# Kernel optimization log

Hardware: AMD Instinct MI355X
Metric: run time of the kernel (lower is better)

The kernel has to match this reference:

```python
import jax, jax.numpy as jnp
import numpy as np

CAPS_N, DIMS_N, ROUNDS = 10, 16, 3
IN_CAPS_N, IN_DIMS_N = 1152, 8
BATCH = 256
EPS = 1e-7  # keras backend.epsilon()


def squash(x, axis=-1):
    sq = jnp.sum(x * x, axis=axis, keepdims=True)
    return (sq / (1.0 + sq)) * x / jnp.sqrt(sq + EPS)


def setup_inputs() -> dict:
    key = jax.random.key(0)
    k1, k2 = jax.random.split(key)
    inputs = jax.random.normal(k1, (BATCH, IN_CAPS_N, IN_DIMS_N), dtype=jnp.float32)
    # glorot-ish scale for the transform weights
    W = jax.random.normal(k2, (CAPS_N, IN_CAPS_N, DIMS_N, IN_DIMS_N), dtype=jnp.float32) * 0.05
    return {"inputs": inputs, "W": W}


def reference(inputs, W):
    # u_hat[b,j,i,d] = W[j,i] @ inputs[b,i]  (per-pair prediction vectors)
    u_hat = jnp.einsum('jide,bie->bjid', W, inputs)  # [B, caps_n, in_caps_n, dims_n]
    B = inputs.shape[0]
    cc = jnp.zeros((B, CAPS_N, IN_CAPS_N), dtype=u_hat.dtype)  # routing logits
    v = None
    for r in range(ROUNDS):
        c = jax.nn.softmax(cc, axis=1)                    # softmax over output capsules
        s = jnp.einsum('bji,bjid->bjd', c, u_hat)         # weighted sum over input caps
        v = squash(s, axis=-1)                            # [B, caps_n, dims_n]
        if r != ROUNDS - 1:
            cc = cc + jnp.einsum('bjid,bjd->bji', u_hat, v)  # agreement
    return v
```

## Files before the change

### kernel.cpp

```cpp
#include <hip/hip_runtime.h>

#define B_N 256
#define IC_N 1152
#define J_N 10
#define D_N 16

typedef __attribute__((ext_vector_type(8))) short short8;
typedef __attribute__((ext_vector_type(4))) float floatx4;

union u4s8 { uint4 u; short8 s; };

__device__ __forceinline__ float bf_lo(unsigned int u){
  union { unsigned int i; float f; } c; c.i = u << 16; return c.f;
}
__device__ __forceinline__ float bf_hi(unsigned int u){
  union { unsigned int i; float f; } c; c.i = u & 0xffff0000u; return c.f;
}
__device__ __forceinline__ unsigned int rne16(float f){
  union { float ff; unsigned int i; } c; c.ff = f;
  return (c.i + 0x7FFFu + ((c.i >> 16) & 1u)) >> 16;
}
__device__ __forceinline__ unsigned int pack_rne(float lo, float hi){
  return rne16(lo) | (rne16(hi) << 16);
}
__device__ __forceinline__ unsigned int pack_trunc(float lo, float hi){
  union { float f; unsigned int u; } a, b; a.f = lo; b.f = hi;
  return __builtin_amdgcn_perm(b.u, a.u, 0x07060302u);
}

__global__ __launch_bounds__(256) void caps_prep(
    const float* __restrict__ W, uint4* __restrict__ wsf,
    uint4* __restrict__ wcc2, float* __restrict__ vsum)
{
  const int tid = threadIdx.x;
  const int t0 = blockIdx.x * 256 + tid;
  if (t0 < B_N * J_N * D_N) vsum[t0] = 0.f;
  __shared__ unsigned int lw[1024];
  const int j = blockIdx.x / 72, itile = blockIdx.x % 72;
  const float4* Wt = (const float4*)(W + ((size_t)(j * IC_N + itile * 16) << 7));
  #pragma unroll
  for (int h = 0; h < 2; ++h) {
    const float4 f = Wt[h * 256 + tid];
    lw[(h * 256 + tid) * 2]     = pack_rne(f.x, f.y);
    lw[(h * 256 + tid) * 2 + 1] = pack_rne(f.z, f.w);
  }
  __syncthreads();
  {
    const int ktl = tid >> 6, ln = tid & 63;
    const int base = (ktl * 4 + (ln >> 4)) * 64 + (ln & 15) * 4;
    uint4 q;
    q.x = lw[base]; q.y = lw[base + 1]; q.z = lw[base + 2]; q.w = lw[base + 3];
    wsf[((size_t)j * 288 + itile * 4 + ktl) * 64 + ln] = q;
  }
  {
    const int e = tid >> 5, lane2 = tid & 31;
    const int il = lane2 & 15, dbase = (lane2 >> 4) * 8;
    unsigned short h[8];
    #pragma unroll
    for (int k = 0; k < 8; ++k) {
      const unsigned int u = lw[il * 64 + (dbase + k) * 4 + (e >> 1)];
      h[k] = (e & 1) ? (unsigned short)(u >> 16) : (unsigned short)(u & 0xffffu);
    }
    uint4 q;
    q.x = h[0] | ((unsigned int)h[1] << 16);
    q.y = h[2] | ((unsigned int)h[3] << 16);
    q.z = h[4] | ((unsigned int)h[5] << 16);
    q.w = h[6] | ((unsigned int)h[7] << 16);
    wcc2[(((size_t)j * 8 + e) * 72 + itile) * 32 + lane2] = q;
  }
}

__global__ __launch_bounds__(640, 5) void caps_pass(
    const float* __restrict__ x,
    const uint4* __restrict__ wsf, const uint4* __restrict__ wcc2,
    const uint4* __restrict__ vsbf, float* __restrict__ s_part, const int round)
{
  __shared__ float ccl[10 * 32 * 17];
  __shared__ unsigned int xt[32 * 17 * 4];

  const int tid  = threadIdx.x;
  const int wave = tid >> 6;
  const int lane = tid & 63;
  const int quad = lane >> 4;
  const int col  = lane & 15;
  const int b0   = blockIdx.x << 4;
  const int i0   = blockIdx.y << 5;

  if (tid < 512) {
    const int b = tid >> 5, j4 = tid & 31;
    const int half = j4 & 1;
    #pragma unroll
    for (int ii = 0; ii < 2; ++ii) {
      const int i = ii * 16 + (j4 >> 1);
      const float4 v = ((const float4*)(x + ((size_t)((b0 + b) * IC_N + i0 + i) << 3)))[half];
      const int idx = ((i * 17 + b) << 2) + (half << 1);
      xt[idx]     = pack_rne(v.x, v.y);
      xt[idx + 1] = pack_rne(v.z, v.w);
    }
  }
  __syncthreads();
  const uint4* xtq = (const uint4*)xt;

  if (round > 0) {
    short8 av = {0,0,0,0,0,0,0,0};
    if (quad < 2)
      av = *(const short8*)&vsbf[((size_t)(b0 + col) * J_N + wave) * 2 + quad];
    #pragma unroll
    for (int c = 0; c < 2; ++c) {
      uint4 bvq[8];
      #pragma unroll
      for (int e = 0; e < 8; ++e) {
        uint4 q = {0u, 0u, 0u, 0u};
        if (lane < 32)
          q = wcc2[(((size_t)wave * 8 + e) * 72 + (blockIdx.y * 2 + c)) * 32 + lane];
        bvq[e] = q;
      }
      uint4 xr[4];
      #pragma unroll
      for (int r = 0; r < 4; ++r)
        xr[r] = xtq[(c * 16 + col) * 17 + quad * 4 + r];
      floatx4 cc4 = {0.f, 0.f, 0.f, 0.f};
      #pragma unroll
      for (int e = 0; e < 8; ++e) {
        u4s8 bv; bv.u = bvq[e];
        floatx4 tf = {0.f, 0.f, 0.f, 0.f};
        tf = __builtin_amdgcn_mfma_f32_16x16x32_bf16(av, bv.s, tf, 0, 0, 0);
        #pragma unroll
        for (int r = 0; r < 4; ++r) {
          const unsigned int u = ((const unsigned int*)&xr[r])[e >> 1];
          const float xe = (e & 1) ? bf_hi(u) : bf_lo(u);
          cc4[r] += tf[r] * xe;
        }
      }
      #pragma unroll
      for (int r = 0; r < 4; ++r)
        ccl[(wave * 32 + c * 16 + col) * 17 + quad * 4 + r] = cc4[r];
    }
    __syncthreads();
    if (tid < 512) {
      const int i = tid >> 4, b = tid & 15;
      float cc[10];
      #pragma unroll
      for (int j = 0; j < 10; ++j) cc[j] = ccl[(j * 32 + i) * 17 + b];
      float m = cc[0];
      #pragma unroll
      for (int j = 1; j < 10; ++j) m = fmaxf(m, cc[j]);
      float den = 0.f;
      #pragma unroll
      for (int j = 0; j < 10; ++j) { cc[j] = __expf(cc[j] - m); den += cc[j]; }
      const float rd = __builtin_amdgcn_rcpf(den);
      #pragma unroll
      for (int j = 0; j < 10; ++j) ccl[(j * 32 + i) * 17 + b] = cc[j] * rd;
    }
    __syncthreads();
  }

  floatx4 acc = {0.f, 0.f, 0.f, 0.f};
  #pragma unroll
  for (int kt = 0; kt < 8; ++kt) {
    const int il = kt * 4 + quad;
    const uint4 xq = xtq[il * 17 + col];
    const uint4 wf = wsf[((size_t)wave * 288 + (blockIdx.y << 3) + kt) * 64 + lane];
    const float c = (round > 0) ? ccl[(wave * 32 + il) * 17 + col] : 0.1f;
    short8 af;
    unsigned int* aq = (unsigned int*)&af;
    aq[0] = pack_trunc(bf_lo(xq.x) * c, bf_hi(xq.x) * c);
    aq[1] = pack_trunc(bf_lo(xq.y) * c, bf_hi(xq.y) * c);
    aq[2] = pack_trunc(bf_lo(xq.z) * c, bf_hi(xq.z) * c);
    aq[3] = pack_trunc(bf_lo(xq.w) * c, bf_hi(xq.w) * c);
    u4s8 bw; bw.u = wf;
    acc = __builtin_amdgcn_mfma_f32_16x16x32_bf16(af, bw.s, acc, 0, 0, 0);
  }
  float* sp = s_part + ((((size_t)blockIdx.x * 10 + wave) * 16 + quad * 4) * 36
                        + blockIdx.y) * 16 + col;
  #pragma unroll
  for (int r = 0; r < 4; ++r) sp[(size_t)r * 36 * 16] = acc[r];
}

__global__ __launch_bounds__(256) void caps_squash(
    const float* __restrict__ s_part, float* __restrict__ vsum,
    unsigned int* __restrict__ vsbf_u, float* __restrict__ out, const int round)
{
  const int tid  = threadIdx.x;
  const int w    = tid >> 6;
  const int lane = tid & 63;
  const int bj   = blockIdx.x * 4 + w;
  const int b    = bj / 10, j = bj - b * 10;
  const int btile = b >> 4, brem = b & 15;
  const float* base = s_part + (((size_t)btile * 10 + j) * 16 + brem) * 576;
  float acc = 0.f;
  #pragma unroll
  for (int q = 0; q < 9; ++q) acc += base[q * 64 + lane];
  acc += __shfl_xor(acc, 16, 64);
  acc += __shfl_xor(acc, 32, 64);
  const float s = acc;
  float sq = s * s;
  sq += __shfl_xor(sq, 1, 16);
  sq += __shfl_xor(sq, 2, 16);
  sq += __shfl_xor(sq, 4, 16);
  sq += __shfl_xor(sq, 8, 16);
  const float coef = (sq / (1.f + sq)) * rsqrtf(sq + 1e-7f);
  const float v = coef * s;
  if (round < 2) {
    const float vprev = (lane < 16) ? vsum[bj * 16 + lane] : 0.f;
    const float vt = vprev + v;
    const float vtn = __shfl_down(vt, 1, 64);
    if (lane < 16) {
      vsum[bj * 16 + lane] = vt;
      if (!(lane & 1))
        vsbf_u[bj * 8 + (lane >> 1)] = pack_rne(vt, vtn);
    }
  } else if (lane < 16) {
    out[bj * 16 + lane] = v;
  }
}

extern "C" void kernel_launch(void* const* d_in, const int* in_sizes, int n_in,
                              void* d_out, int out_size, void* d_ws, size_t ws_size,
                              hipStream_t stream)
{
  const float* x_p = (const float*)d_in[0];
  const float* W_p = (const float*)d_in[1];

  uint4* wsf   = (uint4*)d_ws;
  uint4* wcc2  = wsf + 184320;
  float* s_prt = (float*)(wcc2 + 184320);
  float* vsum  = s_prt + 2949120;
  unsigned int* vsbf_u = (unsigned int*)(vsum + 40960);
  float* out_p = (float*)d_out;

  caps_prep<<<dim3(720), dim3(256), 0, stream>>>(W_p, wsf, wcc2, vsum);
  for (int r = 0; r < 3; ++r) {
    caps_pass<<<dim3(16, 36), dim3(640), 0, stream>>>(
        x_p, wsf, wcc2, (const uint4*)vsbf_u, s_prt, r);
    caps_squash<<<dim3(640), dim3(256), 0, stream>>>(
        s_prt, vsum, vsbf_u, out_p, r);
  }
}
```

Before: 111.3 us.

## Fuse squash into next routing pass and drop intermediate squash launches

Each routing pass now reduces the previous round's partial sums and applies squash itself, building the bf16 agreement operand in shared memory. This removes two intermediate squash kernels and the vsbf staging buffer. Ping-pong partial-sum buffers separate the rounds, and vsum is written once by the blockIdx.y==0 blocks. The cost is that every one of the 36 i-tile blocks redundantly re-reads and re-reduces the same 16x10 slab of partial sums, which greatly increases cache traffic and adds latency before the main MFMA work.

```diff
diff --git a/kernel.cpp b/kernel.cpp
--- a/kernel.cpp
+++ b/kernel.cpp
@@ -30,11 +30,9 @@
 
 __global__ __launch_bounds__(256) void caps_prep(
     const float* __restrict__ W, uint4* __restrict__ wsf,
-    uint4* __restrict__ wcc2, float* __restrict__ vsum)
+    uint4* __restrict__ wcc2)
 {
   const int tid = threadIdx.x;
-  const int t0 = blockIdx.x * 256 + tid;
-  if (t0 < B_N * J_N * D_N) vsum[t0] = 0.f;
   __shared__ unsigned int lw[1024];
   const int j = blockIdx.x / 72, itile = blockIdx.x % 72;
   const float4* Wt = (const float4*)(W + ((size_t)(j * IC_N + itile * 16) << 7));
@@ -73,10 +71,12 @@
 __global__ __launch_bounds__(640, 5) void caps_pass(
     const float* __restrict__ x,
     const uint4* __restrict__ wsf, const uint4* __restrict__ wcc2,
-    const uint4* __restrict__ vsbf, float* __restrict__ s_part, const int round)
+    const float* __restrict__ sp_prev, float* __restrict__ sp_cur,
+    float* __restrict__ vsum, const int round)
 {
   __shared__ float ccl[10 * 32 * 17];
   __shared__ unsigned int xt[32 * 17 * 4];
+  __shared__ float vs_l[10][16 * 17];
 
   const int tid  = threadIdx.x;
   const int wave = tid >> 6;
@@ -98,13 +98,48 @@
       xt[idx + 1] = pack_rne(v.z, v.w);
     }
   }
+
+  short8 av = {0,0,0,0,0,0,0,0};
+  if (round > 0) {
+    const float* slab = sp_prev + ((size_t)(blockIdx.x * 10 + wave) * 16) * 576;
+    #pragma unroll 2
+    for (int b = 0; b < 16; ++b) {
+      const float* pb = slab + b * 576;
+      float a = 0.f;
+      #pragma unroll
+      for (int q = 0; q < 9; ++q) a += pb[q * 64 + lane];
+      a += __shfl_xor(a, 16, 64);
+      a += __shfl_xor(a, 32, 64);
+      const float s = a;
+      float sq = s * s;
+      sq += __shfl_xor(sq, 1, 16);
+      sq += __shfl_xor(sq, 2, 16);
+      sq += __shfl_xor(sq, 4, 16);
+      sq += __shfl_xor(sq, 8, 16);
+      const float coef = (sq / (1.f + sq)) * rsqrtf(sq + 1e-7f);
+      const float v = coef * s;
+      const int bj = (b0 + b) * J_N + wave;
+      float vt = v;
+      if (round == 2) vt += vsum[bj * 16 + col];
+      if (lane < 16) {
+        vs_l[wave][b * 17 + lane] = vt;
+        if (round == 1 && blockIdx.y == 0) vsum[bj * 16 + lane] = vt;
+      }
+    }
+    if (quad < 2) {
+      unsigned int* aq = (unsigned int*)&av;
+      #pragma unroll
+      for (int m = 0; m < 4; ++m) {
+        const float lo = vs_l[wave][col * 17 + quad * 8 + 2 * m];
+        const float hi = vs_l[wave][col * 17 + quad * 8 + 2 * m + 1];
+        aq[m] = pack_rne(lo, hi);
+      }
+    }
+  }
   __syncthreads();
   const uint4* xtq = (const uint4*)xt;
 
   if (round > 0) {
-    short8 av = {0,0,0,0,0,0,0,0};
-    if (quad < 2)
-      av = *(const short8*)&vsbf[((size_t)(b0 + col) * J_N + wave) * 2 + quad];
     #pragma unroll
     for (int c = 0; c < 2; ++c) {
       uint4 bvq[8];
@@ -171,15 +206,14 @@
     u4s8 bw; bw.u = wf;
     acc = __builtin_amdgcn_mfma_f32_16x16x32_bf16(af, bw.s, acc, 0, 0, 0);
   }
-  float* sp = s_part + ((((size_t)blockIdx.x * 10 + wave) * 16 + quad * 4) * 36
+  float* sp = sp_cur + ((((size_t)blockIdx.x * 10 + wave) * 16 + quad * 4) * 36
                         + blockIdx.y) * 16 + col;
   #pragma unroll
   for (int r = 0; r < 4; ++r) sp[(size_t)r * 36 * 16] = acc[r];
 }
 
-__global__ __launch_bounds__(256) void caps_squash(
-    const float* __restrict__ s_part, float* __restrict__ vsum,
-    unsigned int* __restrict__ vsbf_u, float* __restrict__ out, const int round)
+__global__ __launch_bounds__(256) void caps_squash_final(
+    const float* __restrict__ s_part, float* __restrict__ out)
 {
   const int tid  = threadIdx.x;
   const int w    = tid >> 6;
@@ -201,18 +235,7 @@
   sq += __shfl_xor(sq, 8, 16);
   const float coef = (sq / (1.f + sq)) * rsqrtf(sq + 1e-7f);
   const float v = coef * s;
-  if (round < 2) {
-    const float vprev = (lane < 16) ? vsum[bj * 16 + lane] : 0.f;
-    const float vt = vprev + v;
-    const float vtn = __shfl_down(vt, 1, 64);
-    if (lane < 16) {
-      vsum[bj * 16 + lane] = vt;
-      if (!(lane & 1))
-        vsbf_u[bj * 8 + (lane >> 1)] = pack_rne(vt, vtn);
-    }
-  } else if (lane < 16) {
-    out[bj * 16 + lane] = v;
-  }
+  if (lane < 16) out[bj * 16 + lane] = v;
 }
 
 extern "C" void kernel_launch(void* const* d_in, const int* in_sizes, int n_in,
@@ -224,16 +247,17 @@
 
   uint4* wsf   = (uint4*)d_ws;
   uint4* wcc2  = wsf + 184320;
-  float* s_prt = (float*)(wcc2 + 184320);
-  float* vsum  = s_prt + 2949120;
-  unsigned int* vsbf_u = (unsigned int*)(vsum + 40960);
+  float* spA   = (float*)(wcc2 + 184320);
+  float* spB   = spA + 1474560;
+  float* vsum  = spB + 1474560;
   float* out_p = (float*)d_out;
 
-  caps_prep<<<dim3(720), dim3(256), 0, stream>>>(W_p, wsf, wcc2, vsum);
-  for (int r = 0; r < 3; ++r) {
-    caps_pass<<<dim3(16, 36), dim3(640), 0, stream>>>(
-        x_p, wsf, wcc2, (const uint4*)vsbf_u, s_prt, r);
-    caps_squash<<<dim3(640), dim3(256), 0, stream>>>(
-        s_prt, vsum, vsbf_u, out_p, r);
-  }
-}
+  caps_prep<<<dim3(720), dim3(256), 0, stream>>>(W_p, wsf, wcc2);
+  caps_pass<<<dim3(16, 36), dim3(640), 0, stream>>>(
+      x_p, wsf, wcc2, spA, spA, vsum, 0);
+  caps_pass<<<dim3(16, 36), dim3(640), 0, stream>>>(
+      x_p, wsf, wcc2, spA, spB, vsum, 1);
+  caps_pass<<<dim3(16, 36), dim3(640), 0, stream>>>(
+      x_p, wsf, wcc2, spB, spA, vsum, 2);
+  caps_squash_final<<<dim3(640), dim3(256), 0, stream>>>(spA, out_p);
+}
```

After: 153.9 us. 38.2% more time.

## Swizzle pass grid for XCD locality, prefetch W fragments, split MFMA accumulators

Applied to the files above, without the earlier changes.

Flattens the caps_pass grid to 1D and remaps block ids so consecutive blocks on each XCD (bid&7) share the same input-capsule tile. The goal is better L2 reuse of the W fragments. The W fragments for the main MFMA loop are prefetched into registers early, before the barrier in round 0 and after the agreement MFMAs in later rounds, so their latency overlaps other work. The MFMA chain is also split into two accumulators to break the dependency. The costs are higher register pressure from eight held uint4 values under the 640,5 launch bounds, and a possible change in cache behaviour.

```diff
diff --git a/kernel.cpp b/kernel.cpp
--- a/kernel.cpp
+++ b/kernel.cpp
@@ -83,8 +83,13 @@
   const int lane = tid & 63;
   const int quad = lane >> 4;
   const int col  = lane & 15;
-  const int b0   = blockIdx.x << 4;
-  const int i0   = blockIdx.y << 5;
+
+  const int bid = blockIdx.x;
+  const int wid = (bid & 7) * 72 + (bid >> 3);
+  const int bx  = wid & 15;
+  const int by  = wid >> 4;
+  const int b0  = bx << 4;
+  const int i0  = by << 5;
 
   if (tid < 512) {
     const int b = tid >> 5, j4 = tid & 31;
@@ -98,6 +103,13 @@
       xt[idx + 1] = pack_rne(v.z, v.w);
     }
   }
+
+  uint4 wf8[8];
+  if (round == 0) {
+    #pragma unroll
+    for (int kt = 0; kt < 8; ++kt)
+      wf8[kt] = wsf[((size_t)wave * 288 + (by << 3) + kt) * 64 + lane];
+  }
   __syncthreads();
   const uint4* xtq = (const uint4*)xt;
 
@@ -112,7 +124,7 @@
       for (int e = 0; e < 8; ++e) {
         uint4 q = {0u, 0u, 0u, 0u};
         if (lane < 32)
-          q = wcc2[(((size_t)wave * 8 + e) * 72 + (blockIdx.y * 2 + c)) * 32 + lane];
+          q = wcc2[(((size_t)wave * 8 + e) * 72 + (by * 2 + c)) * 32 + lane];
         bvq[e] = q;
       }
       uint4 xr[4];
@@ -136,6 +148,9 @@
       for (int r = 0; r < 4; ++r)
         ccl[(wave * 32 + c * 16 + col) * 17 + quad * 4 + r] = cc4[r];
     }
+    #pragma unroll
+    for (int kt = 0; kt < 8; ++kt)
+      wf8[kt] = wsf[((size_t)wave * 288 + (by << 3) + kt) * 64 + lane];
     __syncthreads();
     if (tid < 512) {
       const int i = tid >> 4, b = tid & 15;
@@ -155,12 +170,12 @@
     __syncthreads();
   }
 
-  floatx4 acc = {0.f, 0.f, 0.f, 0.f};
+  floatx4 acc0 = {0.f, 0.f, 0.f, 0.f};
+  floatx4 acc1 = {0.f, 0.f, 0.f, 0.f};
   #pragma unroll
   for (int kt = 0; kt < 8; ++kt) {
     const int il = kt * 4 + quad;
     const uint4 xq = xtq[il * 17 + col];
-    const uint4 wf = wsf[((size_t)wave * 288 + (blockIdx.y << 3) + kt) * 64 + lane];
     const float c = (round > 0) ? ccl[(wave * 32 + il) * 17 + col] : 0.1f;
     short8 af;
     unsigned int* aq = (unsigned int*)&af;
@@ -168,11 +183,15 @@
     aq[1] = pack_trunc(bf_lo(xq.y) * c, bf_hi(xq.y) * c);
     aq[2] = pack_trunc(bf_lo(xq.z) * c, bf_hi(xq.z) * c);
     aq[3] = pack_trunc(bf_lo(xq.w) * c, bf_hi(xq.w) * c);
-    u4s8 bw; bw.u = wf;
-    acc = __builtin_amdgcn_mfma_f32_16x16x32_bf16(af, bw.s, acc, 0, 0, 0);
-  }
-  float* sp = s_part + ((((size_t)blockIdx.x * 10 + wave) * 16 + quad * 4) * 36
-                        + blockIdx.y) * 16 + col;
+    u4s8 bw; bw.u = wf8[kt];
+    if (kt & 1)
+      acc1 = __builtin_amdgcn_mfma_f32_16x16x32_bf16(af, bw.s, acc1, 0, 0, 0);
+    else
+      acc0 = __builtin_amdgcn_mfma_f32_16x16x32_bf16(af, bw.s, acc0, 0, 0, 0);
+  }
+  const floatx4 acc = acc0 + acc1;
+  float* sp = s_part + ((((size_t)bx * 10 + wave) * 16 + quad * 4) * 36
+                        + by) * 16 + col;
   #pragma unroll
   for (int r = 0; r < 4; ++r) sp[(size_t)r * 36 * 16] = acc[r];
 }
@@ -231,7 +250,7 @@
 
   caps_prep<<<dim3(720), dim3(256), 0, stream>>>(W_p, wsf, wcc2, vsum);
   for (int r = 0; r < 3; ++r) {
-    caps_pass<<<dim3(16, 36), dim3(640), 0, stream>>>(
+    caps_pass<<<dim3(576), dim3(640), 0, stream>>>(
         x_p, wsf, wcc2, (const uint4*)vsbf_u, s_prt, r);
     caps_squash<<<dim3(640), dim3(256), 0, stream>>>(
         s_prt, vsum, vsbf_u, out_p, r);
```

Measured after the change: 110.3 us (median of 3 runs). About the same (-0.9%).
